# Optimization experiments

Measured on AMD Instinct MI355X. Metric: run time of the kernel, lower is better.

Reference implementation:

```python
import jax, jax.numpy as jnp
import numpy as np

B = 262144
P = 0.8
CLS_NUM_LIST = [500, 477, 456, 435, 415, 396, 378, 361, 345, 329, 314, 300, 286, 273, 261, 249, 238, 227, 217, 207, 197, 188, 180, 172, 164, 156, 149, 142, 136, 130, 124, 118, 113, 108, 103, 98, 94, 90, 85, 82, 78, 74, 71, 68, 65, 62, 59, 56, 54, 51, 49, 47, 45, 43, 41, 39, 37, 35, 34, 32, 31, 29, 28, 27, 26, 24, 23, 22, 21, 20, 19, 18, 18, 17, 16, 15, 15, 14, 13, 13, 12, 12, 11, 11, 10, 10, 9, 9, 8, 8, 8, 7, 7, 7, 6, 6, 6, 5, 5, 5]
C = len(CLS_NUM_LIST)


def _build_weight_matrix():
    n = np.asarray(CLS_NUM_LIST, dtype=np.float64).reshape(C, 1)
    wm = (1.0 / n) * n.T            # wm[i, j] = n_j / n_i
    wm[wm > 1] = 1.0
    wm = np.power(wm, P)
    return jnp.asarray(wm, dtype=jnp.float32)


def setup_inputs() -> dict:
    key = jax.random.key(0)
    kx, kt = jax.random.split(key)
    x = jax.random.normal(kx, (B, C), dtype=jnp.float32)
    target = jax.random.randint(kt, (B,), 0, C, dtype=jnp.int64)
    weight_matrix = _build_weight_matrix()                      # [C, C]
    neg_grad = jnp.full((1, C), 1e-06, dtype=jnp.float32)
    pos_grad = jnp.full((1, C), 1e-06, dtype=jnp.float32)
    return {"x": x, "target": target, "weight_matrix": weight_matrix,
            "neg_grad": neg_grad, "pos_grad": pos_grad}


def reference(x, target, weight_matrix, neg_grad, pos_grad):
    bs, num_classes = x.shape
    onehot = jax.nn.one_hot(target, num_classes, dtype=x.dtype)   # [B, C]
    # one_hot @ weight_matrix is algebraically a row gather
    weight = weight_matrix[target]                                # [B, C]
    weighted_x = x + jnp.log(weight)
    log_sm = jax.nn.log_softmax(weighted_x, axis=1)               # stable log(softmax)
    softmax_x = jnp.exp(log_sm)
    # grad-statistic accumulation (detached in the original)
    grad = jnp.abs(softmax_x - onehot)
    neg_grad_new = neg_grad + (grad * (1.0 - onehot)).sum(0)      # [1, C]
    pos_grad_new = pos_grad + (grad * onehot).sum(0)              # [1, C]
    ratio = pos_grad_new / neg_grad_new
    loss = -jnp.sum(onehot * log_sm) / bs
    return loss, neg_grad_new, pos_grad_new, ratio
```

## Files before the change

### kernel.cpp

```cpp
#include <hip/hip_runtime.h>

#define NCLS 100
#define NROWS 262144
#define MAIN_BLOCKS 2048
#define MAIN_THREADS 256
#define NWAVES (MAIN_THREADS / 64)
#define TILE_ROWS 32
#define NTILES 4
#define TILE_F4 (TILE_ROWS * 25)
#define PART_LD MAIN_BLOCKS
#define NPC (2 * NCLS + 1)
#define WS_NEEDED ((size_t)NPC * PART_LD * 4)


#define COMPROW(buf, LGT, VTX, TT) do {                                        \
    float4 e[4];                                                               \
    float sp = 0.f;                                                            \
    _Pragma("unroll")                                                          \
    for (int m = 0; m < 4; ++m) {                                              \
        if (8 * m + k < 25) {                                                  \
            e[m].x = __expf(buf[m].x + fminf(lgn[m].x - (LGT), 0.f));          \
            e[m].y = __expf(buf[m].y + fminf(lgn[m].y - (LGT), 0.f));          \
            e[m].z = __expf(buf[m].z + fminf(lgn[m].z - (LGT), 0.f));          \
            e[m].w = __expf(buf[m].w + fminf(lgn[m].w - (LGT), 0.f));          \
            sp += (e[m].x + e[m].y) + (e[m].z + e[m].w);                       \
        } else {                                                               \
            e[m] = make_float4(0.f, 0.f, 0.f, 0.f);                            \
        }                                                                      \
    }                                                                          \
    float s = sp + __shfl_xor(sp, 1, 64);                                      \
    s += __shfl_xor(s, 2, 64);                                                 \
    s += __shfl_xor(s, 4, 64);                                                 \
    const float inv_s = 1.0f / s;                                              \
    if (k == 0) {                                                              \
        loss_local += __logf(s) - (VTX);                                       \
        const float pt = __expf(VTX) * inv_s;                                  \
        atomicAdd(&lds_q[TT], pt);                                             \
        atomicAdd(&lds_pos[TT], 1.0f - pt);                                    \
    }                                                                          \
    _Pragma("unroll")                                                          \
    for (int m = 0; m < 4; ++m) {                                              \
        if (8 * m + k < 25) {                                                  \
            S4[m].x = fmaf(e[m].x, inv_s, S4[m].x);                            \
            S4[m].y = fmaf(e[m].y, inv_s, S4[m].y);                            \
            S4[m].z = fmaf(e[m].z, inv_s, S4[m].z);                            \
            S4[m].w = fmaf(e[m].w, inv_s, S4[m].w);                            \
        }                                                                      \
    }                                                                          \
} while (0)

#define STAGE(TI) do {                                                         \
    _Pragma("unroll")                                                          \
    for (int i_ = 0; i_ < 4; ++i_) {                                           \
        const int idx_ = i_ * MAIN_THREADS + threadIdx.x;                      \
        if (idx_ < TILE_F4)                                                    \
            lds_x4[idx_] = x4[base_f4 + (TI) * TILE_F4 + idx_];                \
    }                                                                          \
} while (0)

#define COMPTILE(TI) do {                                                      \
    const int t_ = tr[TI];                                                     \
    const float lgt_ = lgt[TI];                                                \
    float4 buf[4];                                                             \
    buf[0] = lds_x4[oct * 25 + k];                                             \
    buf[1] = lds_x4[oct * 25 + 8 + k];                                         \
    buf[2] = lds_x4[oct * 25 + 16 + k];                                        \
    buf[3] = (k == 0) ? lds_x4[oct * 25 + 24]                                  \
                      : make_float4(0.f, 0.f, 0.f, 0.f);                       \
    const float vt_ = lds_xs[oct * NCLS + t_];   \
    COMPROW(buf, lgt_, vt_, t_);                                               \
} while (0)

__global__ __launch_bounds__(MAIN_THREADS, 4)
void seesaw_main(const float* __restrict__ x,
                 const int* __restrict__ target,
                 const float* __restrict__ wm,
                 float* __restrict__ part,
                 float* __restrict__ out,
                 int use_part) {
    __shared__ float4 lds_x4[TILE_F4];
    __shared__ float lds_lgn[NCLS];
    __shared__ float lds_q[NCLS];
    __shared__ float lds_pos[NCLS];
    __shared__ float lds_S[NWAVES][NCLS];
    __shared__ float lds_loss[NWAVES];

    const int lane = threadIdx.x & 63;
    const int wave = threadIdx.x >> 6;
    const int k    = threadIdx.x & 7;
    const int oct  = threadIdx.x >> 3;
    const float* lds_xs = reinterpret_cast<const float*>(lds_x4);
    const float4* x4 = reinterpret_cast<const float4*>(x);
    const size_t base_f4 = (size_t)blockIdx.x * (NTILES * TILE_F4);
    const int row0 = blockIdx.x * (NTILES * TILE_ROWS) + oct;

    int tr[NTILES];
    tr[0] = target[row0];
    tr[1] = target[row0 + TILE_ROWS];
    tr[2] = target[row0 + 2 * TILE_ROWS];
    tr[3] = target[row0 + 3 * TILE_ROWS];

    if (threadIdx.x < NCLS) {
        lds_lgn[threadIdx.x] = __logf(wm[threadIdx.x]);
        lds_q[threadIdx.x] = 0.f;
        lds_pos[threadIdx.x] = 0.f;
    }
    STAGE(0);
    __syncthreads();

    float4 lgn[4];
#pragma unroll
    for (int m = 0; m < 4; ++m) {
        const int g = 8 * m + k;
        if (g < 25) {
            lgn[m].x = lds_lgn[4 * g + 0];
            lgn[m].y = lds_lgn[4 * g + 1];
            lgn[m].z = lds_lgn[4 * g + 2];
            lgn[m].w = lds_lgn[4 * g + 3];
        } else {
            lgn[m] = make_float4(0.f, 0.f, 0.f, 0.f);
        }
    }
    float lgt[NTILES];
    lgt[0] = lds_lgn[tr[0]];
    lgt[1] = lds_lgn[tr[1]];
    lgt[2] = lds_lgn[tr[2]];
    lgt[3] = lds_lgn[tr[3]];

    float4 S4[4];
#pragma unroll
    for (int m = 0; m < 4; ++m) S4[m] = make_float4(0.f, 0.f, 0.f, 0.f);
    float loss_local = 0.0f;

    COMPTILE(0);
    __syncthreads();
    STAGE(1);
    __syncthreads();
    COMPTILE(1);
    __syncthreads();
    STAGE(2);
    __syncthreads();
    COMPTILE(2);
    __syncthreads();
    STAGE(3);
    __syncthreads();
    COMPTILE(3);

#pragma unroll
    for (int m = 0; m < 4; ++m) {
#pragma unroll
        for (int msk = 8; msk <= 32; msk <<= 1) {
            S4[m].x += __shfl_xor(S4[m].x, msk, 64);
            S4[m].y += __shfl_xor(S4[m].y, msk, 64);
            S4[m].z += __shfl_xor(S4[m].z, msk, 64);
            S4[m].w += __shfl_xor(S4[m].w, msk, 64);
        }
    }
#pragma unroll
    for (int msk = 1; msk < 64; msk <<= 1)
        loss_local += __shfl_xor(loss_local, msk, 64);
    if (lane == 0) lds_loss[wave] = loss_local;

    if (lane < 8) {
#pragma unroll
        for (int m = 0; m < 4; ++m) {
            const int g = 8 * m + lane;
            if (g < 25) {
                lds_S[wave][4 * g + 0] = S4[m].x;
                lds_S[wave][4 * g + 1] = S4[m].y;
                lds_S[wave][4 * g + 2] = S4[m].z;
                lds_S[wave][4 * g + 3] = S4[m].w;
            }
        }
    }
    __syncthreads();

    if (use_part) {
        if (threadIdx.x < NCLS) {
            const int j = threadIdx.x;
            float sb = 0.f;
#pragma unroll
            for (int w = 0; w < NWAVES; ++w) sb += lds_S[w][j];
            part[(size_t)j * PART_LD + blockIdx.x] = sb - lds_q[j];
            part[(size_t)(NCLS + j) * PART_LD + blockIdx.x] = lds_pos[j];
        }
        if (threadIdx.x == 0) {
            float l = 0.f;
#pragma unroll
            for (int w = 0; w < NWAVES; ++w) l += lds_loss[w];
            part[(size_t)(2 * NCLS) * PART_LD + blockIdx.x] = l;
        }
    } else {
        if (threadIdx.x < NCLS) {
            const int j = threadIdx.x;
            float sb = 0.f;
#pragma unroll
            for (int w = 0; w < NWAVES; ++w) sb += lds_S[w][j];
            atomicAdd(&out[1 + j], sb - lds_q[j]);
            atomicAdd(&out[1 + NCLS + j], lds_pos[j]);
        }
        if (threadIdx.x == 0) {
            float l = 0.f;
#pragma unroll
            for (int w = 0; w < NWAVES; ++w) l += lds_loss[w];
            atomicAdd(&out[0], l);
        }
    }
}

__global__ void seesaw_tail(const float* __restrict__ part,
                            const float* __restrict__ neg_in,
                            const float* __restrict__ pos_in,
                            float* __restrict__ out) {
    const int c = blockIdx.x;
    __shared__ float redn[NWAVES], redp[NWAVES];
    const int lane = threadIdx.x & 63;
    const int wave = threadIdx.x >> 6;

    float sn = 0.f, sp = 0.f;
    if (c < NCLS) {
        for (int b = threadIdx.x; b < PART_LD; b += MAIN_THREADS) {
            sn += part[(size_t)c * PART_LD + b];
            sp += part[(size_t)(NCLS + c) * PART_LD + b];
        }
    } else {
        for (int b = threadIdx.x; b < PART_LD; b += MAIN_THREADS)
            sn += part[(size_t)(2 * NCLS) * PART_LD + b];
    }
#pragma unroll
    for (int msk = 1; msk < 64; msk <<= 1) {
        sn += __shfl_xor(sn, msk, 64);
        sp += __shfl_xor(sp, msk, 64);
    }
    if (lane == 0) { redn[wave] = sn; redp[wave] = sp; }
    __syncthreads();
    if (threadIdx.x == 0) {
        float tn = 0.f, tp = 0.f;
#pragma unroll
        for (int w = 0; w < NWAVES; ++w) { tn += redn[w]; tp += redp[w]; }
        if (c < NCLS) {
            const float neg = neg_in[c] + tn;
            const float pos = pos_in[c] + tp;
            out[1 + c] = neg;
            out[1 + NCLS + c] = pos;
            out[1 + 2 * NCLS + c] = pos / neg;
        } else {
            out[0] = tn * (1.0f / (float)NROWS);
        }
    }
}

__global__ void seesaw_init(const float* __restrict__ neg_in,
                            const float* __restrict__ pos_in,
                            float* __restrict__ out) {
    int i = threadIdx.x;
    if (i == 0) out[0] = 0.0f;
    if (i < NCLS) {
        out[1 + i] = neg_in[i];
        out[1 + NCLS + i] = pos_in[i];
    }
}

__global__ void seesaw_fin(float* __restrict__ out) {
    int j = threadIdx.x;
    if (j == 0) out[0] *= (1.0f / (float)NROWS);
    if (j < NCLS) out[1 + 2 * NCLS + j] = out[1 + NCLS + j] / out[1 + j];
}

extern "C" void kernel_launch(void* const* d_in, const int* in_sizes, int n_in,
                              void* d_out, int out_size, void* d_ws, size_t ws_size,
                              hipStream_t stream) {
    const float* x      = (const float*)d_in[0];
    const int*   target = (const int*)d_in[1];
    const float* wm     = (const float*)d_in[2];
    const float* neg_in = (const float*)d_in[3];
    const float* pos_in = (const float*)d_in[4];
    float* out  = (float*)d_out;
    float* part = (float*)d_ws;

    if (ws_size >= WS_NEEDED) {
        hipLaunchKernelGGL(seesaw_main, dim3(MAIN_BLOCKS), dim3(MAIN_THREADS), 0, stream,
                           x, target, wm, part, out, 1);
        hipLaunchKernelGGL(seesaw_tail, dim3(NCLS + 1), dim3(MAIN_THREADS), 0, stream,
                           part, neg_in, pos_in, out);
    } else {
        hipLaunchKernelGGL(seesaw_init, dim3(1), dim3(256), 0, stream,
                           neg_in, pos_in, out);
        hipLaunchKernelGGL(seesaw_main, dim3(MAIN_BLOCKS), dim3(MAIN_THREADS), 0, stream,
                           x, target, wm, part, out, 0);
        hipLaunchKernelGGL(seesaw_fin, dim3(1), dim3(128), 0, stream, out);
    }
}
```

Baseline: 36.17 us.

## Double-buffer LDS tiles with async global_load_lds prefetch

Replaces the synchronous register-staged copy of each x tile into a single LDS buffer with two LDS buffers filled by the `__builtin_amdgcn_global_load_lds` direct-to-LDS load. The next tile is issued before the current one is computed, which halves the number of block barriers. The aim is to overlap global memory latency with the exp/softmax work and skip the register round trip. It relies on the barrier forcing completion of the asynchronous LDS writes. It also doubles LDS use per block, which may lower occupancy.

```diff
diff --git a/kernel.cpp b/kernel.cpp
--- a/kernel.cpp
+++ b/kernel.cpp
@@ -49,25 +49,31 @@
     }                                                                          \
 } while (0)
 
-#define STAGE(TI) do {                                                         \
+#define STAGE_GL(DSTBUF, TI) do {                                              \
     _Pragma("unroll")                                                          \
     for (int i_ = 0; i_ < 4; ++i_) {                                           \
         const int idx_ = i_ * MAIN_THREADS + threadIdx.x;                      \
-        if (idx_ < TILE_F4)                                                    \
-            lds_x4[idx_] = x4[base_f4 + (TI) * TILE_F4 + idx_];                \
+        if (idx_ < TILE_F4) {                                                  \
+            __builtin_amdgcn_global_load_lds(                                  \
+                (const __attribute__((address_space(1))) void*)                \
+                    &x4[base_f4 + (size_t)(TI) * TILE_F4 + idx_],              \
+                (__attribute__((address_space(3))) void*)&DSTBUF[idx_],        \
+                16, 0, 0);                                                     \
+        }                                                                      \
     }                                                                          \
 } while (0)
 
-#define COMPTILE(TI) do {                                                      \
+#define COMPTILE(SRCBUF, TI) do {                                              \
     const int t_ = tr[TI];                                                     \
     const float lgt_ = lgt[TI];                                                \
     float4 buf[4];                                                             \
-    buf[0] = lds_x4[oct * 25 + k];                                             \
-    buf[1] = lds_x4[oct * 25 + 8 + k];                                         \
-    buf[2] = lds_x4[oct * 25 + 16 + k];                                        \
-    buf[3] = (k == 0) ? lds_x4[oct * 25 + 24]                                  \
+    buf[0] = SRCBUF[oct * 25 + k];                                             \
+    buf[1] = SRCBUF[oct * 25 + 8 + k];                                         \
+    buf[2] = SRCBUF[oct * 25 + 16 + k];                                        \
+    buf[3] = (k == 0) ? SRCBUF[oct * 25 + 24]                                  \
                       : make_float4(0.f, 0.f, 0.f, 0.f);                       \
-    const float vt_ = lds_xs[oct * NCLS + t_];   \
+    const float vt_ =                                                          \
+        reinterpret_cast<const float*>(SRCBUF)[oct * NCLS + t_];               \
     COMPROW(buf, lgt_, vt_, t_);                                               \
 } while (0)
 
@@ -78,7 +84,8 @@
                  float* __restrict__ part,
                  float* __restrict__ out,
                  int use_part) {
-    __shared__ float4 lds_x4[TILE_F4];
+    __shared__ float4 lds_bufA[TILE_F4];
+    __shared__ float4 lds_bufB[TILE_F4];
     __shared__ float lds_lgn[NCLS];
     __shared__ float lds_q[NCLS];
     __shared__ float lds_pos[NCLS];
@@ -89,10 +96,11 @@
     const int wave = threadIdx.x >> 6;
     const int k    = threadIdx.x & 7;
     const int oct  = threadIdx.x >> 3;
-    const float* lds_xs = reinterpret_cast<const float*>(lds_x4);
     const float4* x4 = reinterpret_cast<const float4*>(x);
     const size_t base_f4 = (size_t)blockIdx.x * (NTILES * TILE_F4);
     const int row0 = blockIdx.x * (NTILES * TILE_ROWS) + oct;
+
+    STAGE_GL(lds_bufA, 0);
 
     int tr[NTILES];
     tr[0] = target[row0];
@@ -105,7 +113,6 @@
         lds_q[threadIdx.x] = 0.f;
         lds_pos[threadIdx.x] = 0.f;
     }
-    STAGE(0);
     __syncthreads();
 
     float4 lgn[4];
@@ -132,19 +139,16 @@
     for (int m = 0; m < 4; ++m) S4[m] = make_float4(0.f, 0.f, 0.f, 0.f);
     float loss_local = 0.0f;
 
-    COMPTILE(0);
-    __syncthreads();
-    STAGE(1);
-    __syncthreads();
-    COMPTILE(1);
-    __syncthreads();
-    STAGE(2);
-    __syncthreads();
-    COMPTILE(2);
-    __syncthreads();
-    STAGE(3);
-    __syncthreads();
-    COMPTILE(3);
+    STAGE_GL(lds_bufB, 1);
+    COMPTILE(lds_bufA, 0);
+    __syncthreads();
+    STAGE_GL(lds_bufA, 2);
+    COMPTILE(lds_bufB, 1);
+    __syncthreads();
+    STAGE_GL(lds_bufB, 3);
+    COMPTILE(lds_bufA, 2);
+    __syncthreads();
+    COMPTILE(lds_bufB, 3);
 
 #pragma unroll
     for (int m = 0; m < 4; ++m) {
```

New measurement: 33.17 us. 8.3% less time.
